# Performance work log

Measured on AMD Instinct MI355X. Metric: run time of the kernel, lower is better.

## Reference

```python
import jax, jax.numpy as jnp
import numpy as np

N_NODES = 8192
N_EDGES = 262144
FEAT = 128


def _lin(key, fan_in, fan_out):
    k1, k2 = jax.random.split(key)
    s = 1.0 / np.sqrt(fan_in)
    w = jax.random.uniform(k1, (fan_in, fan_out), jnp.float32, -s, s)
    b = jax.random.uniform(k2, (fan_out,), jnp.float32, -s, s)
    return w, b


def setup_inputs() -> dict:
    key = jax.random.key(0)
    ks = jax.random.split(key, 16)
    adj = jax.random.randint(ks[0], (2, N_EDGES), 0, N_NODES)
    features = jax.random.normal(ks[1], (N_NODES, FEAT), jnp.float32)
    w1, b1 = _lin(ks[2], FEAT, 64)
    w2, b2 = _lin(ks[3], 64, 32)
    w3, b3 = _lin(ks[4], 32, 32)
    # MultiheadAttention params (embed_dim=32, 1 head)
    kq = jax.random.split(ks[5], 2)
    wqkv = jax.random.uniform(kq[0], (96, 32), jnp.float32, -1/np.sqrt(32), 1/np.sqrt(32))
    bqkv = jnp.zeros((96,), jnp.float32)
    wo = jax.random.uniform(kq[1], (32, 32), jnp.float32, -1/np.sqrt(32), 1/np.sqrt(32))
    bo = jnp.zeros((32,), jnp.float32)
    w4, b4 = _lin(ks[6], 32, 32)
    w5a, b5a = _lin(ks[7], 32, 32)
    w6a, b6a = _lin(ks[8], 32, 64)
    w7a, b7a = _lin(ks[9], 64, 2)
    w5f, b5f = _lin(ks[10], 32, 32)
    w6f, b6f = _lin(ks[11], 32, 64)
    w7f, b7f = _lin(ks[12], 64, FEAT)
    return dict(adj=adj, features=features, w1=w1, b1=b1, w2=w2, b2=b2, w3=w3, b3=b3,
                wqkv=wqkv, bqkv=bqkv, wo=wo, bo=bo, w4=w4, b4=b4,
                w5a=w5a, b5a=b5a, w6a=w6a, b6a=b6a, w7a=w7a, b7a=b7a,
                w5f=w5f, b5f=b5f, w6f=w6f, b6f=b6f, w7f=w7f, b7f=b7f)


def _gcn(x, w, b, src, dst, norm, n):
    # PyG GCNConv: out = scatter_add(norm * (x W)[src] -> dst) + b
    h = x @ w
    return jax.ops.segment_sum(h[src] * norm[:, None], dst, num_segments=n) + b


def reference(adj, features, w1, b1, w2, b2, w3, b3, wqkv, bqkv, wo, bo, w4, b4,
              w5a, b5a, w6a, b6a, w7a, b7a, w5f, b5f, w6f, b6f, w7f, b7f):
    n = features.shape[0]
    loops = jnp.arange(n)
    src = jnp.concatenate([adj[0], loops])  # self-loops added (gcn_norm)
    dst = jnp.concatenate([adj[1], loops])
    deg = jax.ops.segment_sum(jnp.ones_like(src, jnp.float32), dst, num_segments=n)
    dinv = jnp.where(deg > 0, jax.lax.rsqrt(deg), 0.0)
    norm = dinv[src] * dinv[dst]

    h = jax.nn.relu(_gcn(features, w1, b1, src, dst, norm, n))
    h = jax.nn.relu(_gcn(h, w2, b2, src, dst, norm, n))
    h = jax.nn.relu(_gcn(h, w3, b3, src, dst, norm, n))

    # single-head self-attention over all nodes (seq_len=n, batch=1)
    qkv = h @ wqkv.T + bqkv
    q, k, v = jnp.split(qkv, 3, axis=-1)  # [n,32] each
    attn = jax.nn.softmax((q @ k.T) * (1.0 / np.sqrt(32.0)), axis=-1)  # [n,n]
    h = (attn @ v) @ wo.T + bo

    h = jax.nn.relu(_gcn(h, w4, b4, src, dst, norm, n))

    da = jax.nn.relu(_gcn(h, w5a, b5a, src, dst, norm, n))
    da = jax.nn.relu(_gcn(da, w6a, b6a, src, dst, norm, n))
    da = jax.nn.relu(_gcn(da, w7a, b7a, src, dst, norm, n))  # [n,2]

    df = jax.nn.relu(_gcn(h, w5f, b5f, src, dst, norm, n))
    df = jax.nn.relu(_gcn(df, w6f, b6f, src, dst, norm, n))
    df = jax.nn.relu(_gcn(df, w7f, b7f, src, dst, norm, n))  # [n,FEAT]
    return (da, df)
```

## Files before the change

### kernel.cpp

```cpp
#include <hip/hip_runtime.h>

#define N_NODES 8192
#define N_EDGES 262144

typedef __attribute__((ext_vector_type(4))) float f32x4;
typedef _Float16 half8 __attribute__((ext_vector_type(8)));
typedef _Float16 half4v __attribute__((ext_vector_type(4)));
typedef __fp16 fp16x2 __attribute__((ext_vector_type(2)));
union UH { half8 h8; fp16x2 h2[4]; };
union HC { _Float16 h; unsigned short u; };


__global__ void __launch_bounds__(256) zero_kernel(int4* __restrict__ p) {
  p[blockIdx.x * 256 + threadIdx.x] = make_int4(0, 0, 0, 0);
}


__global__ void __launch_bounds__(1024) scan_kernel(const int* __restrict__ cnt,
                                                    int* __restrict__ rp,
                                                    float* __restrict__ dinv,
                                                    int* __restrict__ cur) {
  __shared__ int sums[1024];
  const int t = threadIdx.x;
  const int base = t * 8;
  int c[8];
  int s = 0;
#pragma unroll
  for (int i = 0; i < 8; ++i) { c[i] = cnt[base + i]; s += c[i]; cur[base + i] = 0; }
  sums[t] = s;
  __syncthreads();
  for (int off = 1; off < 1024; off <<= 1) {
    int v = (t >= off) ? sums[t - off] : 0;
    __syncthreads();
    sums[t] += v;
    __syncthreads();
  }
  int run = (t == 0) ? 0 : sums[t - 1];
#pragma unroll
  for (int i = 0; i < 8; ++i) {
    rp[base + i] = run;
    run += c[i];
    dinv[base + i] = rsqrtf((float)(c[i] + 1));
  }
  if (t == 1023) rp[N_NODES] = run;
}

__global__ void __launch_bounds__(256) fill_kernel(const int* __restrict__ src,
                                                   const int* __restrict__ dst,
                                                   const int* __restrict__ rp,
                                                   const float* __restrict__ dinv,
                                                   int* __restrict__ cur,
                                                   int* __restrict__ col,
                                                   float* __restrict__ wgt) {
  int e = blockIdx.x * 256 + threadIdx.x;
  int d = dst[e], s = src[e];
  int p = atomicAdd(&cur[d], 1);
  int at = rp[d] + p;
  col[at] = s;
  wgt[at] = dinv[s] * dinv[d];
}


template <int FIN, int FOUT, bool WT, bool BIAS, bool RELU, bool O16>
__device__ __forceinline__ void mm_body(const float* __restrict__ x,
                                        const float* __restrict__ w,
                                        const float* __restrict__ bias, void* out,
                                        int bx, int tid, float* ws, float* xs) {
  constexpr int VEC = (FOUT >= 32) ? 4 : 1;
  constexpr int TC = FOUT / VEC;
  constexpr int ROWS = 256 / TC;
  const int r0 = bx * ROWS;
  for (int i = tid; i < FIN * FOUT; i += 256) {
    int k = i / FOUT, j = i % FOUT;
    ws[i] = WT ? w[j * FIN + k] : w[i];
  }
  for (int i = tid; i < ROWS * FIN; i += 256) {
    int r = i / FIN, k = i % FIN;
    xs[r * (FIN + 1) + k] = x[(size_t)(r0 + r) * FIN + k];
  }
  __syncthreads();
  const int jc = tid % TC, r = tid / TC;
  float acc[VEC];
#pragma unroll
  for (int v = 0; v < VEC; ++v) acc[v] = 0.0f;
#pragma unroll
  for (int k = 0; k < FIN; ++k) {
    const float xv = xs[r * (FIN + 1) + k];
#pragma unroll
    for (int v = 0; v < VEC; ++v) acc[v] += xv * ws[k * FOUT + jc * VEC + v];
  }
  float oval[VEC];
#pragma unroll
  for (int v = 0; v < VEC; ++v) {
    int j = jc * VEC + v;
    float o = BIAS ? (acc[v] + bias[j]) : acc[v];
    if (RELU) o = fmaxf(o, 0.0f);
    oval[v] = o;
  }
  if constexpr (O16 && VEC == 4) {
    unsigned short* o16 = (unsigned short*)out;
    half4v pk;
#pragma unroll
    for (int v = 0; v < 4; ++v) pk[v] = (_Float16)oval[v];
    *(half4v*)&o16[(size_t)(r0 + r) * FOUT + jc * 4] = pk;
  } else {
    float* of = (float*)out;
#pragma unroll
    for (int v = 0; v < VEC; ++v) of[(size_t)(r0 + r) * FOUT + jc * VEC + v] = oval[v];
  }
}

template <int FIN, int FOUT, bool WT, bool BIAS, bool RELU = false, bool O16 = false>
__global__ void __launch_bounds__(256) mm_kernel(const float* __restrict__ x,
                                                 const float* __restrict__ w,
                                                 const float* __restrict__ bias,
                                                 void* out) {
  constexpr int VEC = (FOUT >= 32) ? 4 : 1;
  constexpr int ROWS = 256 / (FOUT / VEC);
  __shared__ float ws[FIN * FOUT];
  __shared__ float xs[ROWS * (FIN + 1)];
  mm_body<FIN, FOUT, WT, BIAS, RELU, O16>(x, w, bias, out, blockIdx.x, threadIdx.x, ws, xs);
}

template <int FIN, int FOUT, bool WT, bool BIAS, bool RELU, int G, bool O16A = false,
          bool O16B = false>
__global__ void __launch_bounds__(256) mm_dual_kernel(
    const float* __restrict__ xA, const float* __restrict__ wA,
    const float* __restrict__ bA, void* outA,
    const float* __restrict__ xB, const float* __restrict__ wB,
    const float* __restrict__ bB, void* outB) {
  constexpr int VEC = (FOUT >= 32) ? 4 : 1;
  constexpr int ROWS = 256 / (FOUT / VEC);
  __shared__ float ws[FIN * FOUT];
  __shared__ float xs[ROWS * (FIN + 1)];
  if (blockIdx.x < G)
    mm_body<FIN, FOUT, WT, BIAS, RELU, O16A>(xA, wA, bA, outA, blockIdx.x, threadIdx.x, ws, xs);
  else
    mm_body<FIN, FOUT, WT, BIAS, RELU, O16B>(xB, wB, bB, outB, blockIdx.x - G, threadIdx.x, ws,
                                             xs);
}


template <int F, bool BR, bool I16, bool O16>
__device__ __forceinline__ void aggv_body(const void* __restrict__ t,
                                          const int* __restrict__ rp,
                                          const int* __restrict__ col,
                                          const float* __restrict__ wgt,
                                          const float* __restrict__ dinv,
                                          const float* __restrict__ bias,
                                          void* __restrict__ out, int bx, int tid) {
  constexpr int FPL = I16 ? 8 : 4;
  constexpr int TPN = F / FPL;
  constexpr int EPI = 64 / TPN;
  const int wv = tid >> 6;
  const int lane = tid & 63;
  const int n = bx * 4 + wv;
  const int eo = lane / TPN;
  const int fq = lane % TPN;
  const float di = dinv[n];
  const int rs = rp[n], re = rp[n + 1];
  float acc[FPL];
#pragma unroll
  for (int i = 0; i < FPL; ++i) acc[i] = 0.f;

  auto accum = [&](int node, float w) {
    if constexpr (I16) {
      const half8 hv = *(const half8*)((const unsigned short*)t + (size_t)node * F + fq * 8);
#pragma unroll
      for (int i = 0; i < 8; ++i) acc[i] += w * (float)hv[i];
    } else {
      const f32x4 v = *(const f32x4*)((const float*)t + (size_t)node * F + fq * 4);
#pragma unroll
      for (int i = 0; i < 4; ++i) acc[i] += w * v[i];
    }
  };
  if (eo == 0) accum(n, di * di);
  for (int e = rs + eo; e < re; e += EPI) {
    accum(col[e], wgt[e]);
  }
#pragma unroll
  for (int off = TPN; off < 64; off <<= 1) {
#pragma unroll
    for (int i = 0; i < FPL; ++i) acc[i] += __shfl_xor(acc[i], off, 64);
  }
  if (eo == 0) {
    float r[FPL];
#pragma unroll
    for (int i = 0; i < FPL; ++i) {
      float v = acc[i];
      if (BR) v = fmaxf(v + bias[fq * FPL + i], 0.f);
      r[i] = v;
    }
    if constexpr (O16) {
      unsigned short* o = (unsigned short*)out;
      if constexpr (FPL == 8) {
        half8 pk;
#pragma unroll
        for (int i = 0; i < 8; ++i) pk[i] = (_Float16)r[i];
        *(half8*)&o[(size_t)n * F + fq * 8] = pk;
      } else {
        half4v pk;
#pragma unroll
        for (int i = 0; i < 4; ++i) pk[i] = (_Float16)r[i];
        *(half4v*)&o[(size_t)n * F + fq * 4] = pk;
      }
    } else {
      float* o = (float*)out;
#pragma unroll
      for (int i = 0; i < FPL; i += 4)
        *(f32x4*)&o[(size_t)n * F + fq * FPL + i] = f32x4{r[i], r[i + 1], r[i + 2], r[i + 3]};
    }
  }
}

template <int F, bool BR = true, bool I16 = false, bool O16 = false>
__global__ void __launch_bounds__(256) aggv_kernel(const void* __restrict__ t,
                                                   const int* __restrict__ rp,
                                                   const int* __restrict__ col,
                                                   const float* __restrict__ wgt,
                                                   const float* __restrict__ dinv,
                                                   const float* __restrict__ bias,
                                                   void* __restrict__ out) {
  aggv_body<F, BR, I16, O16>(t, rp, col, wgt, dinv, bias, out, blockIdx.x, threadIdx.x);
}

template <int F, bool BR, bool I16, bool O16, int G>
__global__ void __launch_bounds__(256) aggv_dual_kernel(
    const void* __restrict__ tA, const float* __restrict__ bA, void* __restrict__ outA,
    const void* __restrict__ tB, const float* __restrict__ bB, void* __restrict__ outB,
    const int* __restrict__ rp, const int* __restrict__ col,
    const float* __restrict__ wgt, const float* __restrict__ dinv) {
  if (blockIdx.x < G)
    aggv_body<F, BR, I16, O16>(tA, rp, col, wgt, dinv, bA, outA, blockIdx.x, threadIdx.x);
  else
    aggv_body<F, BR, I16, O16>(tB, rp, col, wgt, dinv, bB, outB, blockIdx.x - G, threadIdx.x);
}


__global__ void __launch_bounds__(256) cm_kernel(const int* __restrict__ dst,
                                                 int* __restrict__ cnt,
                                                 const float* __restrict__ feat,
                                                 const float* __restrict__ w1,
                                                 unsigned short* __restrict__ T16) {
  __shared__ float ws[128 * 64];
  __shared__ float xs[16 * 129];
  if (blockIdx.x < 512) {
    mm_body<128, 64, false, false, false, true>(feat, w1, nullptr, T16, blockIdx.x,
                                                threadIdx.x, ws, xs);
  } else {
    int e = (blockIdx.x - 512) * 256 + threadIdx.x;
    atomicAdd(&cnt[dst[e]], 1);
  }
}

__global__ void __launch_bounds__(256) het1_kernel(
    const float* __restrict__ h6a, const float* __restrict__ w7a, float* __restrict__ pre7a,
    const unsigned short* __restrict__ h6f, float* __restrict__ g7f,
    const int* __restrict__ rp, const int* __restrict__ col,
    const float* __restrict__ wgt, const float* __restrict__ dinv) {
  __shared__ float ws[64 * 2];
  __shared__ float xs[128 * 65];
  if (blockIdx.x < 64)
    mm_body<64, 2, false, false, false, false>(h6a, w7a, nullptr, pre7a, blockIdx.x,
                                               threadIdx.x, ws, xs);
  else
    aggv_body<64, false, true, false>(h6f, rp, col, wgt, dinv, nullptr, g7f,
                                      blockIdx.x - 64, threadIdx.x);
}

__global__ void __launch_bounds__(256) het2_kernel(
    const float* __restrict__ pre7a, const float* __restrict__ b7a, float* __restrict__ outa,
    const float* __restrict__ g7f, const float* __restrict__ w7f,
    const float* __restrict__ b7f, float* __restrict__ outf,
    const int* __restrict__ rp, const int* __restrict__ col,
    const float* __restrict__ wgt, const float* __restrict__ dinv) {
  __shared__ float ws[64 * 128];
  __shared__ float xs[8 * 65];
  if (blockIdx.x < 64) {
    const int tid = threadIdx.x;
    const int n = blockIdx.x * 128 + tid / 2;
    const int f = tid & 1;
    const float di = dinv[n];
    float acc = di * di * pre7a[(size_t)n * 2 + f];
    const int rs = rp[n], re = rp[n + 1];
    for (int e = rs; e < re; ++e) {
      acc += wgt[e] * pre7a[(size_t)col[e] * 2 + f];
    }
    acc += b7a[f];
    outa[(size_t)n * 2 + f] = fmaxf(acc, 0.0f);
  } else {
    mm_body<64, 128, false, true, true, false>(g7f, w7f, b7f, outf, blockIdx.x - 64,
                                               threadIdx.x, ws, xs);
  }
}


__global__ void __launch_bounds__(256) qkv_kernel(const float* __restrict__ x,
                                                  const float* __restrict__ wqkv,
                                                  const float* __restrict__ bqkv,
                                                  unsigned short* __restrict__ Q16,
                                                  unsigned short* __restrict__ K16,
                                                  unsigned short* __restrict__ V16) {
  __shared__ float wls[96 * 33];
  __shared__ float xs[8 * 33];
  const int tid = threadIdx.x;
  const int r = tid >> 5, j = tid & 31;
  const int row = blockIdx.x * 8 + r;
  for (int i = tid; i < 96 * 32; i += 256) wls[(i >> 5) * 33 + (i & 31)] = wqkv[i];
  xs[(tid >> 5) * 33 + (tid & 31)] = x[(size_t)(blockIdx.x * 8 + (tid >> 5)) * 32 + (tid & 31)];
  __syncthreads();
  float aq = bqkv[j], ak = bqkv[32 + j], av = bqkv[64 + j];
#pragma unroll
  for (int k = 0; k < 32; ++k) {
    const float xv = xs[r * 33 + k];
    aq += xv * wls[j * 33 + k];
    ak += xv * wls[(32 + j) * 33 + k];
    av += xv * wls[(64 + j) * 33 + k];
  }
  const float QSCALE = 1.4426950408889634f * 0.17677669529663687f;
  aq *= QSCALE;
  HC cq, ck, cv;
  cq.h = (_Float16)aq;
  ck.h = (_Float16)ak;
  cv.h = (_Float16)av;
  Q16[row * 32 + j] = cq.u;
  K16[row * 32 + j] = ck.u;
  const int ko = row & 31;
  const int slot = 8 * ((ko & 15) >> 2) + ((ko >> 4) << 2) + (ko & 3);
  V16[j * N_NODES + (row & ~31) + slot] = cv.u;
}


__device__ __forceinline__ void wave_writeout(float (*lds)[544], float (*wexp)[16],
                                              float* Mq, float* Lq, const f32x4& o1,
                                              const f32x4& o2, float m, float l, int wid,
                                              int g, int li, int tid, int qt, int by,
                                              float* __restrict__ part) {
#pragma unroll
  for (int r = 0; r < 4; ++r) {
    lds[wid][(4 * g + r) * 16 + li] = o1[r];
    lds[wid][(16 + 4 * g + r) * 16 + li] = o2[r];
  }
  if (g == 0) {
    lds[wid][512 + li] = m;
    lds[wid][528 + li] = l;
  }
  __syncthreads();
  if (tid < 16) {
    const int q = tid;
    const float m0 = lds[0][512 + q], m1 = lds[1][512 + q];
    const float m2 = lds[2][512 + q], m3 = lds[3][512 + q];
    const float M = fmaxf(fmaxf(m0, m1), fmaxf(m2, m3));
    const float w0 = exp2f(m0 - M), w1 = exp2f(m1 - M);
    const float w2 = exp2f(m2 - M), w3 = exp2f(m3 - M);
    wexp[0][q] = w0; wexp[1][q] = w1; wexp[2][q] = w2; wexp[3][q] = w3;
    Mq[q] = M;
    Lq[q] = w0 * lds[0][528 + q] + w1 * lds[1][528 + q] +
            w2 * lds[2][528 + q] + w3 * lds[3][528 + q];
  }
  __syncthreads();
  const int base = (qt * 4 + by) * 544;
#pragma unroll
  for (int e2 = 0; e2 < 2; ++e2) {
    const int e = tid + e2 * 256;
    const int q = e & 15;
    part[base + e] = wexp[0][q] * lds[0][e] + wexp[1][q] * lds[1][e] +
                     wexp[2][q] * lds[2][e] + wexp[3][q] * lds[3][e];
  }
  if (tid < 16) {
    part[base + 512 + tid] = Mq[tid];
    part[base + 528 + tid] = Lq[tid];
  }
}

__global__ void __launch_bounds__(256, 4) attn_mfma_kernel(
    const unsigned short* __restrict__ Q16, const unsigned short* __restrict__ K16,
    const unsigned short* __restrict__ V16, float* __restrict__ part) {
  __shared__ float lds[4][544];
  __shared__ float wexp[4][16];
  __shared__ float Mq[16], Lq[16];
  const int tid = threadIdx.x;
  const int wid = tid >> 6;
  const int lane = tid & 63;
  const int g = lane >> 4;
  const int li = lane & 15;
  const int qpair = blockIdx.x;
  const int q0A = qpair * 32;
  const int q0B = q0A + 16;
  const int kbeg = blockIdx.y * 2048 + wid * 512;

  const half8 qfA = *(const half8*)&Q16[(q0A + li) * 32 + 8 * g];
  const half8 qfB = *(const half8*)&Q16[(q0B + li) * 32 + 8 * g];
  const int koff = li * 32 + 8 * g;
  const int vA = li * N_NODES + 8 * g;
  const int vB = (16 + li) * N_NODES + 8 * g;

  f32x4 oAA = {0.f, 0.f, 0.f, 0.f}, oBA = {0.f, 0.f, 0.f, 0.f};
  f32x4 oAB = {0.f, 0.f, 0.f, 0.f}, oBB = {0.f, 0.f, 0.f, 0.f};
  float mA = -1e30f, lA = 0.f, mB = -1e30f, lB = 0.f;

  for (int t = kbeg; t < kbeg + 512; t += 64) {
    const half8 k0 = *(const half8*)&K16[(t)*32 + koff];
    const half8 k1 = *(const half8*)&K16[(t + 16) * 32 + koff];
    const half8 k2 = *(const half8*)&K16[(t + 32) * 32 + koff];
    const half8 k3 = *(const half8*)&K16[(t + 48) * 32 + koff];
    const half8 va0 = *(const half8*)&V16[vA + t];
    const half8 vb0 = *(const half8*)&V16[vB + t];
    const half8 va1 = *(const half8*)&V16[vA + t + 32];
    const half8 vb1 = *(const half8*)&V16[vB + t + 32];

    {
      f32x4 s0 = {0.f, 0.f, 0.f, 0.f}, s1 = {0.f, 0.f, 0.f, 0.f};
      f32x4 s2 = {0.f, 0.f, 0.f, 0.f}, s3 = {0.f, 0.f, 0.f, 0.f};
      s0 = __builtin_amdgcn_mfma_f32_16x16x32_f16(k0, qfA, s0, 0, 0, 0);
      s1 = __builtin_amdgcn_mfma_f32_16x16x32_f16(k1, qfA, s1, 0, 0, 0);
      s2 = __builtin_amdgcn_mfma_f32_16x16x32_f16(k2, qfA, s2, 0, 0, 0);
      s3 = __builtin_amdgcn_mfma_f32_16x16x32_f16(k3, qfA, s3, 0, 0, 0);
      float mxl = fmaxf(fmaxf(fmaxf(s0[0], s0[1]), fmaxf(s0[2], s0[3])),
                        fmaxf(fmaxf(s1[0], s1[1]), fmaxf(s1[2], s1[3])));
      mxl = fmaxf(mxl, fmaxf(fmaxf(fmaxf(s2[0], s2[1]), fmaxf(s2[2], s2[3])),
                             fmaxf(fmaxf(s3[0], s3[1]), fmaxf(s3[2], s3[3]))));
      if (!__all(mxl <= mA)) {
        float mx = mxl;
        mx = fmaxf(mx, __shfl_xor(mx, 16, 64));
        mx = fmaxf(mx, __shfl_xor(mx, 32, 64));
        const float mn = fmaxf(mA, mx);
        const float fct = exp2f(mA - mn);
        oAA *= fct; oBA *= fct; lA *= fct;
        mA = mn;
      }
      const float p0 = exp2f(s0[0] - mA), p1 = exp2f(s0[1] - mA);
      const float p2 = exp2f(s0[2] - mA), p3 = exp2f(s0[3] - mA);
      const float p4 = exp2f(s1[0] - mA), p5 = exp2f(s1[1] - mA);
      const float p6 = exp2f(s1[2] - mA), p7 = exp2f(s1[3] - mA);
      const float p8 = exp2f(s2[0] - mA), p9 = exp2f(s2[1] - mA);
      const float pa = exp2f(s2[2] - mA), pb = exp2f(s2[3] - mA);
      const float pc = exp2f(s3[0] - mA), pd = exp2f(s3[1] - mA);
      const float pe = exp2f(s3[2] - mA), pf = exp2f(s3[3] - mA);
      lA += (((p0 + p1) + (p2 + p3)) + ((p4 + p5) + (p6 + p7))) +
            (((p8 + p9) + (pa + pb)) + ((pc + pd) + (pe + pf)));
      UH ph0, ph1;
      ph0.h2[0] = __builtin_amdgcn_cvt_pkrtz(p0, p1);
      ph0.h2[1] = __builtin_amdgcn_cvt_pkrtz(p2, p3);
      ph0.h2[2] = __builtin_amdgcn_cvt_pkrtz(p4, p5);
      ph0.h2[3] = __builtin_amdgcn_cvt_pkrtz(p6, p7);
      ph1.h2[0] = __builtin_amdgcn_cvt_pkrtz(p8, p9);
      ph1.h2[1] = __builtin_amdgcn_cvt_pkrtz(pa, pb);
      ph1.h2[2] = __builtin_amdgcn_cvt_pkrtz(pc, pd);
      ph1.h2[3] = __builtin_amdgcn_cvt_pkrtz(pe, pf);
      oAA = __builtin_amdgcn_mfma_f32_16x16x32_f16(va0, ph0.h8, oAA, 0, 0, 0);
      oAA = __builtin_amdgcn_mfma_f32_16x16x32_f16(va1, ph1.h8, oAA, 0, 0, 0);
      oBA = __builtin_amdgcn_mfma_f32_16x16x32_f16(vb0, ph0.h8, oBA, 0, 0, 0);
      oBA = __builtin_amdgcn_mfma_f32_16x16x32_f16(vb1, ph1.h8, oBA, 0, 0, 0);
    }
    {
      f32x4 s0 = {0.f, 0.f, 0.f, 0.f}, s1 = {0.f, 0.f, 0.f, 0.f};
      f32x4 s2 = {0.f, 0.f, 0.f, 0.f}, s3 = {0.f, 0.f, 0.f, 0.f};
      s0 = __builtin_amdgcn_mfma_f32_16x16x32_f16(k0, qfB, s0, 0, 0, 0);
      s1 = __builtin_amdgcn_mfma_f32_16x16x32_f16(k1, qfB, s1, 0, 0, 0);
      s2 = __builtin_amdgcn_mfma_f32_16x16x32_f16(k2, qfB, s2, 0, 0, 0);
      s3 = __builtin_amdgcn_mfma_f32_16x16x32_f16(k3, qfB, s3, 0, 0, 0);
      float mxl = fmaxf(fmaxf(fmaxf(s0[0], s0[1]), fmaxf(s0[2], s0[3])),
                        fmaxf(fmaxf(s1[0], s1[1]), fmaxf(s1[2], s1[3])));
      mxl = fmaxf(mxl, fmaxf(fmaxf(fmaxf(s2[0], s2[1]), fmaxf(s2[2], s2[3])),
                             fmaxf(fmaxf(s3[0], s3[1]), fmaxf(s3[2], s3[3]))));
      if (!__all(mxl <= mB)) {
        float mx = mxl;
        mx = fmaxf(mx, __shfl_xor(mx, 16, 64));
        mx = fmaxf(mx, __shfl_xor(mx, 32, 64));
        const float mn = fmaxf(mB, mx);
        const float fct = exp2f(mB - mn);
        oAB *= fct; oBB *= fct; lB *= fct;
        mB = mn;
      }
      const float p0 = exp2f(s0[0] - mB), p1 = exp2f(s0[1] - mB);
      const float p2 = exp2f(s0[2] - mB), p3 = exp2f(s0[3] - mB);
      const float p4 = exp2f(s1[0] - mB), p5 = exp2f(s1[1] - mB);
      const float p6 = exp2f(s1[2] - mB), p7 = exp2f(s1[3] - mB);
      const float p8 = exp2f(s2[0] - mB), p9 = exp2f(s2[1] - mB);
      const float pa = exp2f(s2[2] - mB), pb = exp2f(s2[3] - mB);
      const float pc = exp2f(s3[0] - mB), pd = exp2f(s3[1] - mB);
      const float pe = exp2f(s3[2] - mB), pf = exp2f(s3[3] - mB);
      lB += (((p0 + p1) + (p2 + p3)) + ((p4 + p5) + (p6 + p7))) +
            (((p8 + p9) + (pa + pb)) + ((pc + pd) + (pe + pf)));
      UH ph0, ph1;
      ph0.h2[0] = __builtin_amdgcn_cvt_pkrtz(p0, p1);
      ph0.h2[1] = __builtin_amdgcn_cvt_pkrtz(p2, p3);
      ph0.h2[2] = __builtin_amdgcn_cvt_pkrtz(p4, p5);
      ph0.h2[3] = __builtin_amdgcn_cvt_pkrtz(p6, p7);
      ph1.h2[0] = __builtin_amdgcn_cvt_pkrtz(p8, p9);
      ph1.h2[1] = __builtin_amdgcn_cvt_pkrtz(pa, pb);
      ph1.h2[2] = __builtin_amdgcn_cvt_pkrtz(pc, pd);
      ph1.h2[3] = __builtin_amdgcn_cvt_pkrtz(pe, pf);
      oAB = __builtin_amdgcn_mfma_f32_16x16x32_f16(va0, ph0.h8, oAB, 0, 0, 0);
      oAB = __builtin_amdgcn_mfma_f32_16x16x32_f16(va1, ph1.h8, oAB, 0, 0, 0);
      oBB = __builtin_amdgcn_mfma_f32_16x16x32_f16(vb0, ph0.h8, oBB, 0, 0, 0);
      oBB = __builtin_amdgcn_mfma_f32_16x16x32_f16(vb1, ph1.h8, oBB, 0, 0, 0);
    }
  }

  lA += __shfl_xor(lA, 16, 64);
  lA += __shfl_xor(lA, 32, 64);
  lB += __shfl_xor(lB, 16, 64);
  lB += __shfl_xor(lB, 32, 64);

  wave_writeout(lds, wexp, Mq, Lq, oAA, oBA, mA, lA, wid, g, li, tid, qpair * 2,
                blockIdx.y, part);
  __syncthreads();
  wave_writeout(lds, wexp, Mq, Lq, oAB, oBB, mB, lB, wid, g, li, tid, qpair * 2 + 1,
                blockIdx.y, part);
}


__global__ void __launch_bounds__(256) attn_combine_wo_w4(const float* __restrict__ part,
                                                          const float* __restrict__ wo,
                                                          const float* __restrict__ bo,
                                                          const float* __restrict__ w4,
                                                          unsigned short* __restrict__ T16out) {
  __shared__ float wols[1024];
  __shared__ float w4ls[1024];
  __shared__ float bos[32];
  __shared__ float aos[4][16][33];
  __shared__ float hs[4][16][33];
  const int tid = threadIdx.x;
  for (int i = tid; i < 1024; i += 256) {
    wols[i] = wo[i];
    w4ls[i] = w4[i];
  }
  if (tid < 32) bos[tid] = bo[tid];
  const int wv = tid >> 6, lane = tid & 63;
  const int qt = blockIdx.x * 4 + wv;
  const int q = lane & 15, g = lane >> 4;
  const int pb = qt * 4 * 544;
  const float m0 = part[pb + 512 + q], m1 = part[pb + 544 + 512 + q];
  const float m2 = part[pb + 1088 + 512 + q], m3 = part[pb + 1632 + 512 + q];
  const float M = fmaxf(fmaxf(m0, m1), fmaxf(m2, m3));
  const float w0 = exp2f(m0 - M), w1 = exp2f(m1 - M);
  const float w2 = exp2f(m2 - M), w3 = exp2f(m3 - M);
  const float L = w0 * part[pb + 528 + q] + w1 * part[pb + 544 + 528 + q] +
                  w2 * part[pb + 1088 + 528 + q] + w3 * part[pb + 1632 + 528 + q];
  const float invL = 1.0f / L;
#pragma unroll
  for (int r = 0; r < 8; ++r) {
    const int d = g + 4 * r;
    const int o = d * 16 + q;
    const float ov = w0 * part[pb + o] + w1 * part[pb + 544 + o] +
                     w2 * part[pb + 1088 + o] + w3 * part[pb + 1632 + o];
    aos[wv][q][d] = ov * invL;
  }
  __syncthreads();
#pragma unroll
  for (int r = 0; r < 8; ++r) {
    const int dout = g + 4 * r;
    float acc = bos[dout];
#pragma unroll
    for (int k = 0; k < 32; ++k) acc += aos[wv][q][k] * wols[dout * 32 + k];
    hs[wv][q][dout] = acc;
  }
#pragma unroll
  for (int r = 0; r < 8; ++r) {
    const int dout = g + 4 * r;
    float acc = 0.f;
#pragma unroll
    for (int k = 0; k < 32; ++k) acc += hs[wv][q][k] * w4ls[k * 32 + dout];
    HC c;
    c.h = (_Float16)acc;
    T16out[(size_t)(qt * 16 + q) * 32 + dout] = c.u;
  }
}


extern "C" void kernel_launch(void* const* d_in, const int* in_sizes, int n_in,
                              void* d_out, int out_size, void* d_ws, size_t ws_size,
                              hipStream_t stream) {
  (void)in_sizes; (void)n_in; (void)out_size; (void)ws_size;
  const int* adj = (const int*)d_in[0];
  const float* feat = (const float*)d_in[1];
  const float* w1 = (const float*)d_in[2];  const float* b1 = (const float*)d_in[3];
  const float* w2 = (const float*)d_in[4];  const float* b2 = (const float*)d_in[5];
  const float* w3 = (const float*)d_in[6];  const float* b3 = (const float*)d_in[7];
  const float* wqkv = (const float*)d_in[8];const float* bqkv = (const float*)d_in[9];
  const float* wo = (const float*)d_in[10]; const float* bo = (const float*)d_in[11];
  const float* w4 = (const float*)d_in[12]; const float* b4 = (const float*)d_in[13];
  const float* w5a = (const float*)d_in[14];const float* b5a = (const float*)d_in[15];
  const float* w6a = (const float*)d_in[16];const float* b6a = (const float*)d_in[17];
  const float* w7a = (const float*)d_in[18];const float* b7a = (const float*)d_in[19];
  const float* w5f = (const float*)d_in[20];const float* b5f = (const float*)d_in[21];
  const float* w6f = (const float*)d_in[22];const float* b6f = (const float*)d_in[23];
  const float* w7f = (const float*)d_in[24];const float* b7f = (const float*)d_in[25];
  float* outp = (float*)d_out;

  float* wsf = (float*)d_ws;
  int* wsi = (int*)d_ws;
  int* cnt = wsi;
  int* cur = wsi + 8192;
  int* rp = wsi + 16384;
  float* dinv = wsf + 24832;
  float* wgt = wsf + 33024;
  int* col = wsi + 295168;
  float* T = wsf + 557312;
  float* T2 = T + 262144;
  float* B0 = wsf + 1605888;
  float* B1 = wsf + 2130176;
  float* B2 = wsf + 2392320;
  unsigned short* Q16 = (unsigned short*)(wsf + 2916608);
  unsigned short* K16 = Q16 + 262144;
  unsigned short* V16 = K16 + 262144;
  unsigned short* T16 = (unsigned short*)T;
  unsigned short* B0h = (unsigned short*)B0;
  unsigned short* B1h = (unsigned short*)B1;
  unsigned short* B2h = (unsigned short*)B2;
  float* part = T;

  const int* src = adj;
  const int* dst = adj + N_EDGES;

  zero_kernel<<<8, 256, 0, stream>>>((int4*)cnt);
  cm_kernel<<<1536, 256, 0, stream>>>(dst, cnt, feat, w1, T16);
  scan_kernel<<<1, 1024, 0, stream>>>(cnt, rp, dinv, cur);
  fill_kernel<<<N_EDGES / 256, 256, 0, stream>>>(src, dst, rp, dinv, cur, col, wgt);

  aggv_kernel<64, true, true, false><<<N_NODES / 4, 256, 0, stream>>>(T16, rp, col, wgt,
                                                                      dinv, b1, B0);
  mm_kernel<64, 32, false, false, false, true><<<N_NODES / 32, 256, 0, stream>>>(
      B0, w2, nullptr, T16);
  aggv_kernel<32, true, true, false><<<N_NODES / 4, 256, 0, stream>>>(T16, rp, col, wgt,
                                                                      dinv, b2, B1);
  mm_kernel<32, 32, false, false, false, true><<<N_NODES / 32, 256, 0, stream>>>(
      B1, w3, nullptr, T16);
  aggv_kernel<32, true, true, false><<<N_NODES / 4, 256, 0, stream>>>(T16, rp, col, wgt,
                                                                      dinv, b3, B0);

  qkv_kernel<<<N_NODES / 8, 256, 0, stream>>>(B0, wqkv, bqkv, Q16, K16, V16);
  {
    dim3 grid(256, 4);
    attn_mfma_kernel<<<grid, 256, 0, stream>>>(Q16, K16, V16, part);
  }
  attn_combine_wo_w4<<<128, 256, 0, stream>>>(part, wo, bo, w4, T16);

  aggv_kernel<32, true, true, true><<<N_NODES / 4, 256, 0, stream>>>(T16, rp, col, wgt,
                                                                     dinv, b4, B0h);

  aggv_kernel<32, false, true, false><<<N_NODES / 4, 256, 0, stream>>>(B0h, rp, col, wgt,
                                                                       dinv, nullptr, T);
  mm_dual_kernel<32, 32, false, true, true, 256, true, true><<<512, 256, 0, stream>>>(
      T, w5a, b5a, B1h, T, w5f, b5f, B2h);
  aggv_dual_kernel<32, false, true, false, 2048><<<4096, 256, 0, stream>>>(
      B1h, nullptr, T, B2h, nullptr, T2, rp, col, wgt, dinv);
  mm_dual_kernel<32, 64, false, true, true, 512, false, true><<<1024, 256, 0, stream>>>(
      T, w6a, b6a, B0, T2, w6f, b6f, B2h);
  het1_kernel<<<64 + 2048, 256, 0, stream>>>(B0, w7a, B1, B2h, T, rp, col, wgt, dinv);
  het2_kernel<<<64 + 1024, 256, 0, stream>>>(B1, b7a, outp, T, w7f, b7f, outp + 16384, rp,
                                             col, wgt, dinv);
}
```

Before: 179.4 us.

## Fuse neighbor aggregation with following dense transform into per-layer kernels

```diff
diff --git a/kernel.cpp b/kernel.cpp
--- a/kernel.cpp
+++ b/kernel.cpp
@@ -110,36 +110,52 @@
   }
 }
 
-template <int FIN, int FOUT, bool WT, bool BIAS, bool RELU = false, bool O16 = false>
-__global__ void __launch_bounds__(256) mm_kernel(const float* __restrict__ x,
-                                                 const float* __restrict__ w,
-                                                 const float* __restrict__ bias,
-                                                 void* out) {
-  constexpr int VEC = (FOUT >= 32) ? 4 : 1;
-  constexpr int ROWS = 256 / (FOUT / VEC);
-  __shared__ float ws[FIN * FOUT];
-  __shared__ float xs[ROWS * (FIN + 1)];
-  mm_body<FIN, FOUT, WT, BIAS, RELU, O16>(x, w, bias, out, blockIdx.x, threadIdx.x, ws, xs);
-}
-
-template <int FIN, int FOUT, bool WT, bool BIAS, bool RELU, int G, bool O16A = false,
-          bool O16B = false>
-__global__ void __launch_bounds__(256) mm_dual_kernel(
-    const float* __restrict__ xA, const float* __restrict__ wA,
-    const float* __restrict__ bA, void* outA,
-    const float* __restrict__ xB, const float* __restrict__ wB,
-    const float* __restrict__ bB, void* outB) {
-  constexpr int VEC = (FOUT >= 32) ? 4 : 1;
-  constexpr int ROWS = 256 / (FOUT / VEC);
-  __shared__ float ws[FIN * FOUT];
-  __shared__ float xs[ROWS * (FIN + 1)];
-  if (blockIdx.x < G)
-    mm_body<FIN, FOUT, WT, BIAS, RELU, O16A>(xA, wA, bA, outA, blockIdx.x, threadIdx.x, ws, xs);
-  else
-    mm_body<FIN, FOUT, WT, BIAS, RELU, O16B>(xB, wB, bB, outB, blockIdx.x - G, threadIdx.x, ws,
-                                             xs);
-}
-
+
+template <int FIN, bool I16, bool GBR>
+__device__ __forceinline__ void gather_row(const void* __restrict__ t,
+                                           const int* __restrict__ rp,
+                                           const int* __restrict__ col,
+                                           const float* __restrict__ wgt,
+                                           const float* __restrict__ dinv,
+                                           const float* __restrict__ gbias,
+                                           float* __restrict__ xrow, int n, int lane) {
+  constexpr int FPL = I16 ? 8 : 4;
+  constexpr int TPN = FIN / FPL;
+  constexpr int EPI = 64 / TPN;
+  const int eo = lane / TPN;
+  const int fq = lane % TPN;
+  const float di = dinv[n];
+  const int rs = rp[n], re = rp[n + 1];
+  float acc[FPL];
+#pragma unroll
+  for (int i = 0; i < FPL; ++i) acc[i] = 0.f;
+  auto accum = [&](int node, float w) {
+    if constexpr (I16) {
+      const half8 hv = *(const half8*)((const unsigned short*)t + (size_t)node * FIN + fq * 8);
+#pragma unroll
+      for (int i = 0; i < 8; ++i) acc[i] += w * (float)hv[i];
+    } else {
+      const f32x4 v = *(const f32x4*)((const float*)t + (size_t)node * FIN + fq * 4);
+#pragma unroll
+      for (int i = 0; i < 4; ++i) acc[i] += w * v[i];
+    }
+  };
+  if (eo == 0) accum(n, di * di);
+  for (int e = rs + eo; e < re; e += EPI) accum(col[e], wgt[e]);
+#pragma unroll
+  for (int off = TPN; off < 64; off <<= 1) {
+#pragma unroll
+    for (int i = 0; i < FPL; ++i) acc[i] += __shfl_xor(acc[i], off, 64);
+  }
+  if (eo == 0) {
+#pragma unroll
+    for (int i = 0; i < FPL; ++i) {
+      float v = acc[i];
+      if (GBR) v = fmaxf(v + gbias[fq * FPL + i], 0.f);
+      xrow[fq * FPL + i] = v;
+    }
+  }
+}
 
 template <int F, bool BR, bool I16, bool O16>
 __device__ __forceinline__ void aggv_body(const void* __restrict__ t,
@@ -162,7 +178,6 @@
   float acc[FPL];
 #pragma unroll
   for (int i = 0; i < FPL; ++i) acc[i] = 0.f;
-
   auto accum = [&](int node, float w) {
     if constexpr (I16) {
       const half8 hv = *(const half8*)((const unsigned short*)t + (size_t)node * F + fq * 8);
@@ -175,9 +190,7 @@
     }
   };
   if (eo == 0) accum(n, di * di);
-  for (int e = rs + eo; e < re; e += EPI) {
-    accum(col[e], wgt[e]);
-  }
+  for (int e = rs + eo; e < re; e += EPI) accum(col[e], wgt[e]);
 #pragma unroll
   for (int off = TPN; off < 64; off <<= 1) {
 #pragma unroll
@@ -193,16 +206,15 @@
     }
     if constexpr (O16) {
       unsigned short* o = (unsigned short*)out;
-      if constexpr (FPL == 8) {
-        half8 pk;
-#pragma unroll
-        for (int i = 0; i < 8; ++i) pk[i] = (_Float16)r[i];
-        *(half8*)&o[(size_t)n * F + fq * 8] = pk;
-      } else {
-        half4v pk;
-#pragma unroll
-        for (int i = 0; i < 4; ++i) pk[i] = (_Float16)r[i];
-        *(half4v*)&o[(size_t)n * F + fq * 4] = pk;
+      half8 pk;
+#pragma unroll
+      for (int i = 0; i < 8; ++i) pk[i] = (_Float16)r[i];
+      if constexpr (FPL == 8) *(half8*)&o[(size_t)n * F + fq * 8] = pk;
+      else {
+        half4v p4;
+#pragma unroll
+        for (int i = 0; i < 4; ++i) p4[i] = (_Float16)r[i];
+        *(half4v*)&o[(size_t)n * F + fq * 4] = p4;
       }
     } else {
       float* o = (float*)out;
@@ -224,16 +236,144 @@
   aggv_body<F, BR, I16, O16>(t, rp, col, wgt, dinv, bias, out, blockIdx.x, threadIdx.x);
 }
 
-template <int F, bool BR, bool I16, bool O16, int G>
-__global__ void __launch_bounds__(256) aggv_dual_kernel(
-    const void* __restrict__ tA, const float* __restrict__ bA, void* __restrict__ outA,
-    const void* __restrict__ tB, const float* __restrict__ bB, void* __restrict__ outB,
+
+template <int FIN, int FOUT, bool GBR, bool PBIAS, bool PRELU, bool O16>
+__device__ __forceinline__ void layer_body(const unsigned short* __restrict__ tin,
+                                           const float* __restrict__ w,
+                                           const float* __restrict__ gbias,
+                                           const float* __restrict__ pbias,
+                                           void* __restrict__ out, const int* rp,
+                                           const int* col, const float* wgt,
+                                           const float* dinv, int bx, int tid, float* ws,
+                                           float* xrow) {
+  for (int i = tid; i < FIN * FOUT; i += 256) ws[i] = w[i];
+  const int wv = tid >> 6, lane = tid & 63;
+  const int n0 = bx * 4;
+  gather_row<FIN, true, GBR>(tin, rp, col, wgt, dinv, gbias, xrow + wv * FIN, n0 + wv, lane);
+  __syncthreads();
+  for (int idx = tid; idx < 4 * FOUT; idx += 256) {
+    const int nn = idx / FOUT, j = idx % FOUT;
+    float acc = PBIAS ? pbias[j] : 0.f;
+    const float* xr = xrow + nn * FIN;
+#pragma unroll
+    for (int k = 0; k < FIN; ++k) acc += xr[k] * ws[k * FOUT + j];
+    if (PRELU) acc = fmaxf(acc, 0.f);
+    if constexpr (O16) {
+      HC c;
+      c.h = (_Float16)acc;
+      ((unsigned short*)out)[(size_t)(n0 + nn) * FOUT + j] = c.u;
+    } else {
+      ((float*)out)[(size_t)(n0 + nn) * FOUT + j] = acc;
+    }
+  }
+}
+
+template <int FIN, int FOUT, bool GBR, bool PBIAS, bool PRELU, bool O16>
+__global__ void __launch_bounds__(256) layer_kernel(const unsigned short* __restrict__ tin,
+                                                    const float* __restrict__ w,
+                                                    const float* __restrict__ gbias,
+                                                    const float* __restrict__ pbias,
+                                                    void* __restrict__ out,
+                                                    const int* __restrict__ rp,
+                                                    const int* __restrict__ col,
+                                                    const float* __restrict__ wgt,
+                                                    const float* __restrict__ dinv) {
+  __shared__ float ws[FIN * FOUT];
+  __shared__ float xrow[4 * FIN];
+  layer_body<FIN, FOUT, GBR, PBIAS, PRELU, O16>(tin, w, gbias, pbias, out, rp, col, wgt,
+                                                dinv, blockIdx.x, threadIdx.x, ws, xrow);
+}
+
+__global__ void __launch_bounds__(256) agg_qkv_kernel(
+    const unsigned short* __restrict__ t3, const float* __restrict__ b3,
+    const float* __restrict__ wqkv, const float* __restrict__ bqkv,
+    unsigned short* __restrict__ Q16, unsigned short* __restrict__ K16,
+    unsigned short* __restrict__ V16, const int* __restrict__ rp,
+    const int* __restrict__ col, const float* __restrict__ wgt,
+    const float* __restrict__ dinv) {
+  __shared__ float ws[32 * 96];
+  __shared__ float xrow[4 * 32];
+  const int tid = threadIdx.x;
+  for (int i = tid; i < 3072; i += 256) {
+    int k = i / 96, j = i % 96;
+    ws[i] = wqkv[j * 32 + k];
+  }
+  const int wv = tid >> 6, lane = tid & 63;
+  const int n0 = blockIdx.x * 4;
+  gather_row<32, true, true>(t3, rp, col, wgt, dinv, b3, xrow + wv * 32, n0 + wv, lane);
+  __syncthreads();
+  const float QSCALE = 1.4426950408889634f * 0.17677669529663687f;
+  for (int idx = tid; idx < 384; idx += 256) {
+    const int nn = idx / 96, j = idx % 96;
+    const int row = n0 + nn;
+    const float* xr = xrow + nn * 32;
+    float acc = bqkv[j];
+#pragma unroll
+    for (int k = 0; k < 32; ++k) acc += xr[k] * ws[k * 96 + j];
+    HC c;
+    if (j < 32) {
+      c.h = (_Float16)(acc * QSCALE);
+      Q16[(size_t)row * 32 + j] = c.u;
+    } else if (j < 64) {
+      c.h = (_Float16)acc;
+      K16[(size_t)row * 32 + (j - 32)] = c.u;
+    } else {
+      c.h = (_Float16)acc;
+      const int ko = row & 31;
+      const int slot = 8 * ((ko & 15) >> 2) + ((ko >> 4) << 2) + (ko & 3);
+      V16[(size_t)(j - 64) * N_NODES + (row & ~31) + slot] = c.u;
+    }
+  }
+}
+
+__global__ void __launch_bounds__(256) layer5_kernel(
+    const unsigned short* __restrict__ h4, const float* __restrict__ w5a,
+    const float* __restrict__ b5a, unsigned short* __restrict__ h5a,
+    const float* __restrict__ w5f, const float* __restrict__ b5f,
+    unsigned short* __restrict__ h5f, const int* __restrict__ rp,
+    const int* __restrict__ col, const float* __restrict__ wgt,
+    const float* __restrict__ dinv) {
+  __shared__ float ws[2048];
+  __shared__ float xrow[4 * 32];
+  const int tid = threadIdx.x;
+  for (int i = tid; i < 1024; i += 256) {
+    ws[i] = w5a[i];
+    ws[1024 + i] = w5f[i];
+  }
+  const int wv = tid >> 6, lane = tid & 63;
+  const int n0 = blockIdx.x * 4;
+  gather_row<32, true, false>(h4, rp, col, wgt, dinv, nullptr, xrow + wv * 32, n0 + wv, lane);
+  __syncthreads();
+  const int nn = tid >> 6;
+  const int j = tid & 63;
+  const int side = j >> 5, jj = j & 31;
+  const float* xr = xrow + nn * 32;
+  const float* wsd = ws + side * 1024;
+  float acc = side ? b5f[jj] : b5a[jj];
+#pragma unroll
+  for (int k = 0; k < 32; ++k) acc += xr[k] * wsd[k * 32 + jj];
+  acc = fmaxf(acc, 0.f);
+  HC c;
+  c.h = (_Float16)acc;
+  unsigned short* o = side ? h5f : h5a;
+  o[(size_t)(n0 + nn) * 32 + jj] = c.u;
+}
+
+__global__ void __launch_bounds__(256) layer6_kernel(
+    const unsigned short* __restrict__ h5a, const float* __restrict__ w6a,
+    const float* __restrict__ b6a, float* __restrict__ h6a,
+    const unsigned short* __restrict__ h5f, const float* __restrict__ w6f,
+    const float* __restrict__ b6f, unsigned short* __restrict__ h6f,
     const int* __restrict__ rp, const int* __restrict__ col,
     const float* __restrict__ wgt, const float* __restrict__ dinv) {
-  if (blockIdx.x < G)
-    aggv_body<F, BR, I16, O16>(tA, rp, col, wgt, dinv, bA, outA, blockIdx.x, threadIdx.x);
+  __shared__ float ws[32 * 64];
+  __shared__ float xrow[4 * 32];
+  if (blockIdx.x < 2048)
+    layer_body<32, 64, false, true, true, false>(h5a, w6a, nullptr, b6a, h6a, rp, col, wgt,
+                                                 dinv, blockIdx.x, threadIdx.x, ws, xrow);
   else
-    aggv_body<F, BR, I16, O16>(tB, rp, col, wgt, dinv, bB, outB, blockIdx.x - G, threadIdx.x);
+    layer_body<32, 64, false, true, true, true>(h5f, w6f, nullptr, b6f, h6f, rp, col, wgt,
+                                                dinv, blockIdx.x - 2048, threadIdx.x, ws, xrow);
 }
 
 
@@ -292,42 +432,6 @@
     mm_body<64, 128, false, true, true, false>(g7f, w7f, b7f, outf, blockIdx.x - 64,
                                                threadIdx.x, ws, xs);
   }
-}
-
-
-__global__ void __launch_bounds__(256) qkv_kernel(const float* __restrict__ x,
-                                                  const float* __restrict__ wqkv,
-                                                  const float* __restrict__ bqkv,
-                                                  unsigned short* __restrict__ Q16,
-                                                  unsigned short* __restrict__ K16,
-                                                  unsigned short* __restrict__ V16) {
-  __shared__ float wls[96 * 33];
-  __shared__ float xs[8 * 33];
-  const int tid = threadIdx.x;
-  const int r = tid >> 5, j = tid & 31;
-  const int row = blockIdx.x * 8 + r;
-  for (int i = tid; i < 96 * 32; i += 256) wls[(i >> 5) * 33 + (i & 31)] = wqkv[i];
-  xs[(tid >> 5) * 33 + (tid & 31)] = x[(size_t)(blockIdx.x * 8 + (tid >> 5)) * 32 + (tid & 31)];
-  __syncthreads();
-  float aq = bqkv[j], ak = bqkv[32 + j], av = bqkv[64 + j];
-#pragma unroll
-  for (int k = 0; k < 32; ++k) {
-    const float xv = xs[r * 33 + k];
-    aq += xv * wls[j * 33 + k];
-    ak += xv * wls[(32 + j) * 33 + k];
-    av += xv * wls[(64 + j) * 33 + k];
-  }
-  const float QSCALE = 1.4426950408889634f * 0.17677669529663687f;
-  aq *= QSCALE;
-  HC cq, ck, cv;
-  cq.h = (_Float16)aq;
-  ck.h = (_Float16)ak;
-  cv.h = (_Float16)av;
-  Q16[row * 32 + j] = cq.u;
-  K16[row * 32 + j] = ck.u;
-  const int ko = row & 31;
-  const int slot = 8 * ((ko & 15) >> 2) + ((ko >> 4) << 2) + (ko & 3);
-  V16[j * N_NODES + (row & ~31) + slot] = cv.u;
 }
 
 
@@ -599,57 +703,54 @@
   float* wgt = wsf + 33024;
   int* col = wsi + 295168;
   float* T = wsf + 557312;
-  float* T2 = T + 262144;
   float* B0 = wsf + 1605888;
   float* B1 = wsf + 2130176;
   float* B2 = wsf + 2392320;
   unsigned short* Q16 = (unsigned short*)(wsf + 2916608);
   unsigned short* K16 = Q16 + 262144;
   unsigned short* V16 = K16 + 262144;
-  unsigned short* T16 = (unsigned short*)T;
+  unsigned short* T16u = (unsigned short*)T;
+  unsigned short* t1 = T16u;
+  unsigned short* t2 = T16u + 524288;
+  unsigned short* t3 = T16u;
+  unsigned short* t4 = (unsigned short*)B2;
   unsigned short* B0h = (unsigned short*)B0;
   unsigned short* B1h = (unsigned short*)B1;
   unsigned short* B2h = (unsigned short*)B2;
+  unsigned short* h6f = T16u;
+  float* g7f = T + 262144;
+  float* pre7a = B1;
   float* part = T;
 
   const int* src = adj;
   const int* dst = adj + N_EDGES;
 
   zero_kernel<<<8, 256, 0, stream>>>((int4*)cnt);
-  cm_kernel<<<1536, 256, 0, stream>>>(dst, cnt, feat, w1, T16);
+  cm_kernel<<<1536, 256, 0, stream>>>(dst, cnt, feat, w1, t1);
   scan_kernel<<<1, 1024, 0, stream>>>(cnt, rp, dinv, cur);
   fill_kernel<<<N_EDGES / 256, 256, 0, stream>>>(src, dst, rp, dinv, cur, col, wgt);
 
-  aggv_kernel<64, true, true, false><<<N_NODES / 4, 256, 0, stream>>>(T16, rp, col, wgt,
-                                                                      dinv, b1, B0);
-  mm_kernel<64, 32, false, false, false, true><<<N_NODES / 32, 256, 0, stream>>>(
-      B0, w2, nullptr, T16);
-  aggv_kernel<32, true, true, false><<<N_NODES / 4, 256, 0, stream>>>(T16, rp, col, wgt,
-                                                                      dinv, b2, B1);
-  mm_kernel<32, 32, false, false, false, true><<<N_NODES / 32, 256, 0, stream>>>(
-      B1, w3, nullptr, T16);
-  aggv_kernel<32, true, true, false><<<N_NODES / 4, 256, 0, stream>>>(T16, rp, col, wgt,
-                                                                      dinv, b3, B0);
-
-  qkv_kernel<<<N_NODES / 8, 256, 0, stream>>>(B0, wqkv, bqkv, Q16, K16, V16);
+  layer_kernel<64, 32, true, false, false, true><<<N_NODES / 4, 256, 0, stream>>>(
+      t1, w2, b1, nullptr, t2, rp, col, wgt, dinv);
+  layer_kernel<32, 32, true, false, false, true><<<N_NODES / 4, 256, 0, stream>>>(
+      t2, w3, b2, nullptr, t3, rp, col, wgt, dinv);
+  agg_qkv_kernel<<<N_NODES / 4, 256, 0, stream>>>(t3, b3, wqkv, bqkv, Q16, K16, V16, rp,
+                                                  col, wgt, dinv);
+
   {
     dim3 grid(256, 4);
     attn_mfma_kernel<<<grid, 256, 0, stream>>>(Q16, K16, V16, part);
   }
-  attn_combine_wo_w4<<<128, 256, 0, stream>>>(part, wo, bo, w4, T16);
-
-  aggv_kernel<32, true, true, true><<<N_NODES / 4, 256, 0, stream>>>(T16, rp, col, wgt,
+  attn_combine_wo_w4<<<128, 256, 0, stream>>>(part, wo, bo, w4, t4);
+
+  aggv_kernel<32, true, true, true><<<N_NODES / 4, 256, 0, stream>>>(t4, rp, col, wgt,
                                                                      dinv, b4, B0h);
 
-  aggv_kernel<32, false, true, false><<<N_NODES / 4, 256, 0, stream>>>(B0h, rp, col, wgt,
-                                                                       dinv, nullptr, T);
-  mm_dual_kernel<32, 32, false, true, true, 256, true, true><<<512, 256, 0, stream>>>(
-      T, w5a, b5a, B1h, T, w5f, b5f, B2h);
-  aggv_dual_kernel<32, false, true, false, 2048><<<4096, 256, 0, stream>>>(
-      B1h, nullptr, T, B2h, nullptr, T2, rp, col, wgt, dinv);
-  mm_dual_kernel<32, 64, false, true, true, 512, false, true><<<1024, 256, 0, stream>>>(
-      T, w6a, b6a, B0, T2, w6f, b6f, B2h);
-  het1_kernel<<<64 + 2048, 256, 0, stream>>>(B0, w7a, B1, B2h, T, rp, col, wgt, dinv);
-  het2_kernel<<<64 + 1024, 256, 0, stream>>>(B1, b7a, outp, T, w7f, b7f, outp + 16384, rp,
-                                             col, wgt, dinv);
-}
+  layer5_kernel<<<N_NODES / 4, 256, 0, stream>>>(B0h, w5a, b5a, B1h, w5f, b5f, B2h, rp,
+                                                 col, wgt, dinv);
+  layer6_kernel<<<2 * (N_NODES / 4), 256, 0, stream>>>(B1h, w6a, b6a, B0, B2h, w6f, b6f,
+                                                       h6f, rp, col, wgt, dinv);
+  het1_kernel<<<64 + 2048, 256, 0, stream>>>(B0, w7a, pre7a, h6f, g7f, rp, col, wgt, dinv);
+  het2_kernel<<<64 + 1024, 256, 0, stream>>>(pre7a, b7a, outp, g7f, w7f, b7f, outp + 16384,
+                                             rp, col, wgt, dinv);
+}
```

Result: no change. 178.0 us (-0.8%).
